# Kernel tuning notes

Hardware: AMD Instinct MI355X
Metric: run time of the kernel (lower is better)

The kernel has to match this reference:

```python
import jax, jax.numpy as jnp
import numpy as np

N_GRAPHS = 1000
P = 300                 # nodes per ring graph
N = N_GRAPHS * P        # 300000 nodes
IN_DIM = 2
HID = 128
OUT_DIM = 2


def _ring_edges():
    idx = jnp.arange(N)
    g = idx // P
    pos = idx % P
    nxt = g * P + (pos + 1) % P
    src = jnp.concatenate([idx, nxt])
    dst = jnp.concatenate([nxt, idx])
    return jnp.stack([src, dst]), g


def setup_inputs() -> dict:
    key = jax.random.key(0)
    ks = jax.random.split(key, 11)
    edge_index, batch = _ring_edges()
    x = jax.random.normal(ks[0], (N, IN_DIM), jnp.float32)

    def glorot(k, fan_in, fan_out):
        lim = np.sqrt(6.0 / (fan_in + fan_out)).astype(np.float32)
        return jax.random.uniform(k, (fan_in, fan_out), jnp.float32, -lim, lim)

    return {
        "x": x,
        "edge_index": edge_index,
        "batch": batch,
        "W1": glorot(ks[1], IN_DIM, HID), "b1": jnp.zeros((HID,), jnp.float32),
        "W2": glorot(ks[2], HID, HID),    "b2": jnp.zeros((HID,), jnp.float32),
        "W3": glorot(ks[3], HID, HID),    "b3": jnp.zeros((HID,), jnp.float32),
        "fw1": glorot(ks[4], HID, HID),   "fb1": jnp.zeros((HID,), jnp.float32),
        "fw2": glorot(ks[5], HID, OUT_DIM), "fb2": jnp.zeros((OUT_DIM,), jnp.float32),
    }


def _gcn_conv(x, W, b, src, dst, norm):
    h = x @ W                              # [N, out]
    msg = h[src] * norm[:, None]           # gather + per-edge scale
    agg = jax.ops.segment_sum(msg, dst, num_segments=N)  # scatter-add
    return agg + b


def reference(x, edge_index, batch, W1, b1, W2, b2, W3, b3, fw1, fb1, fw2, fb2):
    loop = jnp.arange(N)
    src = jnp.concatenate([edge_index[0], loop])
    dst = jnp.concatenate([edge_index[1], loop])
    deg = jax.ops.segment_sum(jnp.ones_like(dst, jnp.float32), dst, num_segments=N)
    dis = jax.lax.rsqrt(deg)               # deg >= 1 due to self-loops
    norm = dis[src] * dis[dst]             # per-edge normalization

    h = jax.nn.relu(_gcn_conv(x, W1, b1, src, dst, norm))
    h = jax.nn.relu(_gcn_conv(h, W2, b2, src, dst, norm))
    h = jax.nn.relu(_gcn_conv(h, W3, b3, src, dst, norm))

    # global mean pool per graph
    sums = jax.ops.segment_sum(h, batch, num_segments=N_GRAPHS)
    cnts = jax.ops.segment_sum(jnp.ones((N,), jnp.float32), batch, num_segments=N_GRAPHS)
    pooled = sums / cnts[:, None]

    out = jax.nn.relu(pooled @ fw1 + fb1)
    out = out @ fw2 + fb2
    return out
```

## Files before the change

kernel.cpp:

```cpp
#include <hip/hip_runtime.h>
#include <hip/hip_bf16.h>
#include <stdint.h>

#define P    300
#define HID  128
#define NG   1000
#define NTL  19

typedef __attribute__((ext_vector_type(8))) short bf16x8;
typedef __attribute__((ext_vector_type(4))) float f32x4;

__device__ short g_wsw[2 * HID * HID];

__device__ __forceinline__ short f2bf(float f) {
    union { float f; uint32_t u; } v; v.f = f;
    uint32_t r = v.u + 0x7fffu + ((v.u >> 16) & 1u);
    return (short)(r >> 16);
}
__device__ __forceinline__ uint32_t pkbf2(float a, float b) {
    union { __hip_bfloat162 h; uint32_t u; } cv;
    cv.h = __float22bfloat162_rn(float2{a, b});
    return cv.u;
}

__global__ __launch_bounds__(256) void k_prep(const float* __restrict__ W2,
                                              const float* __restrict__ W3) {
    int b = blockIdx.x;
    const float* W = (b < 8) ? W2 : W3;
    short* dst = g_wsw + ((b < 8) ? 0 : HID * HID);
    int t    = (b & 7) * 256 + threadIdx.x;
    int fkey = t >> 4;
    int kc   = t & 15;
    bf16x8 o;
    #pragma unroll
    for (int j = 0; j < 8; ++j)
        o[j] = f2bf(W[(kc * 8 + j) * HID + fkey]);
    *(bf16x8*)&dst[(fkey * 16 + (kc ^ (fkey & 15))) * 8] = o;
}

__device__ __forceinline__ void avg_epi(const f32x4 &G, float vp0, float vn3,
                                        float b, float* o) {
    o[0] = (vp0  + G[0] + G[1]) * (1.0f / 3.0f) + b;
    o[1] = (G[0] + G[1] + G[2]) * (1.0f / 3.0f) + b;
    o[2] = (G[1] + G[2] + G[3]) * (1.0f / 3.0f) + b;
    o[3] = (G[2] + G[3] + vn3 ) * (1.0f / 3.0f) + b;
    #pragma unroll
    for (int i = 0; i < 4; ++i) o[i] = o[i] > 0.f ? o[i] : 0.f;
}

template<int POOL>
__device__ __forceinline__ void run_pass(short* __restrict__ buf,
                                         const short* __restrict__ wbase,
                                         const float* __restrict__ bias,
                                         float* __restrict__ pool, int tid) {
    const int lane = tid & 63, wv = tid >> 6, q = lane >> 4, lm = lane & 15;
    const int fkey = wv * 16 + lm;
    bf16x8 wf[4];
    #pragma unroll
    for (int kk = 0; kk < 4; ++kk)
        wf[kk] = *(const bf16x8*)&wbase[(fkey * 16 + ((4 * kk + q) ^ lm)) * 8];
    const float biaf = bias[fkey];
    const int kcs = fkey >> 3, offs = fkey & 7;
    const int sA = (q == 0) ? (48 + lm) : (lane - 16);
    const int sB = (lane + 16) & 63;

    float psum = 0.f;

    auto mfma_tile = [&](int t, f32x4 &G) {
        const short* tb = buf + t * 2048;
        G = f32x4{0.f, 0.f, 0.f, 0.f};
        #pragma unroll
        for (int kk = 0; kk < 4; ++kk) {
            bf16x8 af = *(const bf16x8*)&tb[(lm * 16 + ((4 * kk + q) ^ lm)) * 8];
            G = __builtin_amdgcn_mfma_f32_16x16x32_bf16(af, wf[kk], G, 0, 0, 0);
        }
    };
    auto store_rows = [&](int T, float (&o)[4]) {
        uint32_t u01 = pkbf2(o[0], o[1]);
        uint32_t u23 = pkbf2(o[2], o[3]);
        int n0 = T * 16 + q * 4;
        buf[(n0 * 16       + (kcs ^ ( n0      & 15))) * 8 + offs] = (short)u01;
        buf[((n0 + 1) * 16 + (kcs ^ ((n0 + 1) & 15))) * 8 + offs] = (short)(u01 >> 16);
        buf[((n0 + 2) * 16 + (kcs ^ ((n0 + 2) & 15))) * 8 + offs] = (short)u23;
        buf[((n0 + 3) * 16 + (kcs ^ ((n0 + 3) & 15))) * 8 + offs] = (short)(u23 >> 16);
    };
    auto accum = [&](float (&o)[4]) { psum += o[0] + o[1] + o[2] + o[3]; };

    float c15;
    auto epi_mid = [&](const f32x4 &E, float N0, float (&o)[4]) {
        float vA = __shfl(E[3], sA, 64);
        float vB = __shfl(E[0], sB, 64);
        float vC = __shfl(N0, lm, 64);
        float vp0 = (q == 0) ? c15 : vA;
        float vn3 = (q == 3) ? vC : vB;
        avg_epi(E, vp0, vn3, biaf, o);
        c15 = vA;
    };

    f32x4 GH[10];
    f32x4 GL[9];

    #pragma unroll
    for (int k = 0; k < 9; ++k) mfma_tile(10 + k, GH[k]);
    mfma_tile(0, GH[9]);
    if (!POOL) __syncthreads();

    #pragma unroll
    for (int i = 0; i < 9; ++i) {
        mfma_tile(9 - i, GL[i]);
        if (i == 0) c15 = __shfl(GL[0][3], 48 + lm, 64);
        if (i < 8) {
            float o[4];
            epi_mid(GH[i], GH[i + 1][0], o);
            if (POOL) accum(o); else store_rows(10 + i, o);
        } else {
            float o18[4];
            {
                float vA = __shfl(GH[8][3], sA, 64);
                float vB = __shfl(GH[8][0], sB, 64);
                float vZ = __shfl(GH[9][0], lm, 64);
                float vp0 = (q == 0) ? c15 : vA;
                float vn3 = (q == 2) ? vZ : vB;
                avg_epi(GH[8], vp0, vn3, biaf, o18);
            }
            if (q < 3) { if (POOL) accum(o18); else store_rows(18, o18); }
            float o0[4];
            {
                float vA0 = __shfl(GH[9][3], (lane - 16) & 63, 64);
                float vB0 = __shfl(GH[9][0], sB, 64);
                float vP  = __shfl(GH[8][3], 32 + lm, 64);
                float vN  = __shfl(GL[8][0], lm, 64);
                float vp0 = (q == 0) ? vP : vA0;
                float vn3 = (q == 3) ? vN : vB0;
                avg_epi(GH[9], vp0, vn3, biaf, o0);
            }
            if (POOL) accum(o0); else store_rows(0, o0);
        }
    }
    if (!POOL) __syncthreads();

    c15 = __shfl(GH[9][3], 48 + lm, 64);
    #pragma unroll
    for (int T = 1; T <= 9; ++T) {
        float o[4];
        float N0 = (T < 9) ? GL[8 - T][0] : GH[0][0];
        epi_mid(GL[9 - T], N0, o);
        if (POOL) accum(o); else store_rows(T, o);
    }

    if (POOL) {
        psum += __shfl_xor(psum, 16, 64);
        psum += __shfl_xor(psum, 32, 64);
        if (q == 0) pool[fkey] = psum;
    }
}

__global__ __launch_bounds__(512, 2) void k_graph(
        const float* __restrict__ x,
        const float* __restrict__ W1,  const float* __restrict__ b1,
        const float* __restrict__ b2v, const float* __restrict__ b3v,
        const float* __restrict__ fw1, const float* __restrict__ fb1,
        const float* __restrict__ fw2, const float* __restrict__ fb2,
        float* __restrict__ out) {
    __shared__ __align__(16) short buf[304 * HID];
    __shared__ __align__(16) float scr[640];
    float* xs    = scr;
    float* pool  = scr;
    float* parts = scr + 128;
    float* s1    = scr + 384;

    const int g = blockIdx.x, tid = threadIdx.x;

    if (tid < 150) *(float4*)&xs[tid * 4] = *(const float4*)&x[g * 600 + tid * 4];
    __syncthreads();

    {
        const int kc1 = tid & 15;
        const int n0  = tid >> 4;
        float w1x[8], w1y[8], b1v[8];
        #pragma unroll
        for (int j = 0; j < 8; ++j) {
            w1x[j] = W1[kc1 * 8 + j];
            w1y[j] = W1[HID + kc1 * 8 + j];
            b1v[j] = b1[kc1 * 8 + j];
        }
        #pragma unroll
        for (int it = 0; it < 10; ++it) {
            int node = it * 32 + n0;
            if (node < 304) {
                uint32_t w[4] = {0u, 0u, 0u, 0u};
                if (node < P) {
                    int prev = (node == 0)     ? P - 1 : node - 1;
                    int next = (node == P - 1) ? 0     : node + 1;
                    float2 xp = *(const float2*)&xs[2 * prev];
                    float2 xc = *(const float2*)&xs[2 * node];
                    float2 xn = *(const float2*)&xs[2 * next];
                    float ax = (xp.x + xc.x + xn.x) * (1.f / 3.f);
                    float ay = (xp.y + xc.y + xn.y) * (1.f / 3.f);
                    #pragma unroll
                    for (int jj = 0; jj < 4; ++jj) {
                        float va = ax * w1x[2*jj]   + ay * w1y[2*jj]   + b1v[2*jj];
                        float vb = ax * w1x[2*jj+1] + ay * w1y[2*jj+1] + b1v[2*jj+1];
                        va = va > 0.f ? va : 0.f;
                        vb = vb > 0.f ? vb : 0.f;
                        w[jj] = pkbf2(va, vb);
                    }
                }
                *(uint4*)&buf[(node * 16 + (kc1 ^ (node & 15))) * 8] =
                    uint4{w[0], w[1], w[2], w[3]};
            }
        }
    }
    __syncthreads();

    run_pass<0>(buf, g_wsw,             b2v, pool, tid);
    __syncthreads();
    run_pass<1>(buf, g_wsw + HID * HID, b3v, pool, tid);
    __syncthreads();

    if (tid < 256) {
        int f = tid & 127, half = tid >> 7;
        float p = 0.f;
        const float* fw1c = fw1 + f;
        #pragma unroll 4
        for (int k = half * 64; k < half * 64 + 64; ++k)
            p += pool[k] * fw1c[k * 128];
        parts[half * 128 + f] = p;
    }
    __syncthreads();
    if (tid < 128) {
        float o1 = fb1[tid] + (parts[tid] + parts[128 + tid]) * (1.0f / 300.0f);
        s1[tid] = o1 > 0.f ? o1 : 0.f;
    }
    __syncthreads();
    if (tid < 128) {
        int o = tid >> 6, ln = tid & 63;
        float v = s1[ln] * fw2[ln * 2 + o] + s1[ln + 64] * fw2[(ln + 64) * 2 + o];
        #pragma unroll
        for (int off = 1; off <= 32; off <<= 1)
            v += __shfl_xor(v, off, 64);
        if (ln == 0) out[g * 2 + o] = v + fb2[o];
    }
}

extern "C" void kernel_launch(void* const* d_in, const int* in_sizes, int n_in,
                              void* d_out, int out_size, void* d_ws, size_t ws_size,
                              hipStream_t stream) {
    const float* x   = (const float*)d_in[0];
    const float* W1  = (const float*)d_in[3];
    const float* b1  = (const float*)d_in[4];
    const float* W2  = (const float*)d_in[5];
    const float* b2  = (const float*)d_in[6];
    const float* W3  = (const float*)d_in[7];
    const float* b3  = (const float*)d_in[8];
    const float* fw1 = (const float*)d_in[9];
    const float* fb1 = (const float*)d_in[10];
    const float* fw2 = (const float*)d_in[11];
    const float* fb2 = (const float*)d_in[12];
    float* out = (float*)d_out;

    k_prep <<<dim3(16), dim3(256), 0, stream>>>(W2, W3);
    k_graph<<<dim3(NG), dim3(512), 0, stream>>>(x, W1, b1, b2, b3,
                                                fw1, fb1, fw2, fb2, out);
}
```

Measured before the change: 121.6 us.

## Split each ring graph across two blocks with halo rows and separate FC kernel

```diff
diff --git a/kernel.cpp b/kernel.cpp
--- a/kernel.cpp
+++ b/kernel.cpp
@@ -5,12 +5,13 @@
 #define P    300
 #define HID  128
 #define NG   1000
-#define NTL  19
+#define HR   160
 
 typedef __attribute__((ext_vector_type(8))) short bf16x8;
 typedef __attribute__((ext_vector_type(4))) float f32x4;
 
 __device__ short g_wsw[2 * HID * HID];
+__device__ float g_pool[NG * 2 * HID];
 
 __device__ __forceinline__ short f2bf(float f) {
     union { float f; uint32_t u; } v; v.f = f;
@@ -48,7 +49,7 @@
     for (int i = 0; i < 4; ++i) o[i] = o[i] > 0.f ? o[i] : 0.f;
 }
 
-template<int POOL>
+template<int POOL, int LO, int HI>
 __device__ __forceinline__ void run_pass(short* __restrict__ buf,
                                          const short* __restrict__ wbase,
                                          const float* __restrict__ bias,
@@ -78,15 +79,24 @@
     auto store_rows = [&](int T, float (&o)[4]) {
         uint32_t u01 = pkbf2(o[0], o[1]);
         uint32_t u23 = pkbf2(o[2], o[3]);
-        int n0 = T * 16 + q * 4;
-        buf[(n0 * 16       + (kcs ^ ( n0      & 15))) * 8 + offs] = (short)u01;
-        buf[((n0 + 1) * 16 + (kcs ^ ((n0 + 1) & 15))) * 8 + offs] = (short)(u01 >> 16);
-        buf[((n0 + 2) * 16 + (kcs ^ ((n0 + 2) & 15))) * 8 + offs] = (short)u23;
-        buf[((n0 + 3) * 16 + (kcs ^ ((n0 + 3) & 15))) * 8 + offs] = (short)(u23 >> 16);
-    };
-    auto accum = [&](float (&o)[4]) { psum += o[0] + o[1] + o[2] + o[3]; };
-
-    float c15;
+        int r0 = T * 16 + q * 4;
+        if (r0     >= LO && r0     <= HI)
+            buf[(r0 * 16       + (kcs ^ ( r0      & 15))) * 8 + offs] = (short)u01;
+        if (r0 + 1 >= LO && r0 + 1 <= HI)
+            buf[((r0 + 1) * 16 + (kcs ^ ((r0 + 1) & 15))) * 8 + offs] = (short)(u01 >> 16);
+        if (r0 + 2 >= LO && r0 + 2 <= HI)
+            buf[((r0 + 2) * 16 + (kcs ^ ((r0 + 2) & 15))) * 8 + offs] = (short)u23;
+        if (r0 + 3 >= LO && r0 + 3 <= HI)
+            buf[((r0 + 3) * 16 + (kcs ^ ((r0 + 3) & 15))) * 8 + offs] = (short)(u23 >> 16);
+    };
+    auto accum = [&](int T, float (&o)[4]) {
+        int r0 = T * 16 + q * 4;
+        #pragma unroll
+        for (int i = 0; i < 4; ++i)
+            if (r0 + i >= LO && r0 + i <= HI) psum += o[i];
+    };
+
+    float c15 = 0.f;
     auto epi_mid = [&](const f32x4 &E, float N0, float (&o)[4]) {
         float vA = __shfl(E[3], sA, 64);
         float vB = __shfl(E[0], sB, 64);
@@ -97,55 +107,31 @@
         c15 = vA;
     };
 
-    f32x4 GH[10];
-    f32x4 GL[9];
-
-    #pragma unroll
-    for (int k = 0; k < 9; ++k) mfma_tile(10 + k, GH[k]);
-    mfma_tile(0, GH[9]);
+    f32x4 GH[5];
+    f32x4 GL[5];
+
+    #pragma unroll
+    for (int k = 0; k < 5; ++k) mfma_tile(5 + k, GH[k]);
     if (!POOL) __syncthreads();
 
     #pragma unroll
-    for (int i = 0; i < 9; ++i) {
-        mfma_tile(9 - i, GL[i]);
+    for (int i = 0; i < 5; ++i) {
+        mfma_tile(4 - i, GL[i]);
         if (i == 0) c15 = __shfl(GL[0][3], 48 + lm, 64);
-        if (i < 8) {
-            float o[4];
-            epi_mid(GH[i], GH[i + 1][0], o);
-            if (POOL) accum(o); else store_rows(10 + i, o);
-        } else {
-            float o18[4];
-            {
-                float vA = __shfl(GH[8][3], sA, 64);
-                float vB = __shfl(GH[8][0], sB, 64);
-                float vZ = __shfl(GH[9][0], lm, 64);
-                float vp0 = (q == 0) ? c15 : vA;
-                float vn3 = (q == 2) ? vZ : vB;
-                avg_epi(GH[8], vp0, vn3, biaf, o18);
-            }
-            if (q < 3) { if (POOL) accum(o18); else store_rows(18, o18); }
-            float o0[4];
-            {
-                float vA0 = __shfl(GH[9][3], (lane - 16) & 63, 64);
-                float vB0 = __shfl(GH[9][0], sB, 64);
-                float vP  = __shfl(GH[8][3], 32 + lm, 64);
-                float vN  = __shfl(GL[8][0], lm, 64);
-                float vp0 = (q == 0) ? vP : vA0;
-                float vn3 = (q == 3) ? vN : vB0;
-                avg_epi(GH[9], vp0, vn3, biaf, o0);
-            }
-            if (POOL) accum(o0); else store_rows(0, o0);
-        }
+        float o[4];
+        float N0 = (i < 4) ? GH[i + 1][0] : GH[4][0];
+        epi_mid(GH[i], N0, o);
+        if (POOL) accum(5 + i, o); else store_rows(5 + i, o);
     }
     if (!POOL) __syncthreads();
 
-    c15 = __shfl(GH[9][3], 48 + lm, 64);
-    #pragma unroll
-    for (int T = 1; T <= 9; ++T) {
+    c15 = 0.f;
+    #pragma unroll
+    for (int k = 0; k < 5; ++k) {
         float o[4];
-        float N0 = (T < 9) ? GL[8 - T][0] : GH[0][0];
-        epi_mid(GL[9 - T], N0, o);
-        if (POOL) accum(o); else store_rows(T, o);
+        float N0 = (k < 4) ? GL[3 - k][0] : GH[0][0];
+        epi_mid(GL[4 - k], N0, o);
+        if (POOL) accum(k, o); else store_rows(k, o);
     }
 
     if (POOL) {
@@ -158,20 +144,19 @@
 __global__ __launch_bounds__(512, 2) void k_graph(
         const float* __restrict__ x,
         const float* __restrict__ W1,  const float* __restrict__ b1,
-        const float* __restrict__ b2v, const float* __restrict__ b3v,
-        const float* __restrict__ fw1, const float* __restrict__ fb1,
-        const float* __restrict__ fw2, const float* __restrict__ fb2,
-        float* __restrict__ out) {
-    __shared__ __align__(16) short buf[304 * HID];
-    __shared__ __align__(16) float scr[640];
-    float* xs    = scr;
-    float* pool  = scr;
-    float* parts = scr + 128;
-    float* s1    = scr + 384;
-
-    const int g = blockIdx.x, tid = threadIdx.x;
-
-    if (tid < 150) *(float4*)&xs[tid * 4] = *(const float4*)&x[g * 600 + tid * 4];
+        const float* __restrict__ b2v, const float* __restrict__ b3v) {
+    __shared__ __align__(16) short buf[HR * HID];
+    __shared__ __align__(16) float xs[316];
+    const int bid = blockIdx.x, g = bid >> 1, half = bid & 1;
+    const int tid = threadIdx.x;
+    const int start = half * 150;
+
+    if (tid < 156) {
+        int gn = start - 3 + tid;
+        gn += (gn < 0) ? P : 0;
+        gn -= (gn >= P) ? P : 0;
+        *(float2*)&xs[2 * tid] = *(const float2*)&x[g * 600 + gn * 2];
+    }
     __syncthreads();
 
     {
@@ -185,62 +170,57 @@
             b1v[j] = b1[kc1 * 8 + j];
         }
         #pragma unroll
-        for (int it = 0; it < 10; ++it) {
-            int node = it * 32 + n0;
-            if (node < 304) {
-                uint32_t w[4] = {0u, 0u, 0u, 0u};
-                if (node < P) {
-                    int prev = (node == 0)     ? P - 1 : node - 1;
-                    int next = (node == P - 1) ? 0     : node + 1;
-                    float2 xp = *(const float2*)&xs[2 * prev];
-                    float2 xc = *(const float2*)&xs[2 * node];
-                    float2 xn = *(const float2*)&xs[2 * next];
-                    float ax = (xp.x + xc.x + xn.x) * (1.f / 3.f);
-                    float ay = (xp.y + xc.y + xn.y) * (1.f / 3.f);
-                    #pragma unroll
-                    for (int jj = 0; jj < 4; ++jj) {
-                        float va = ax * w1x[2*jj]   + ay * w1y[2*jj]   + b1v[2*jj];
-                        float vb = ax * w1x[2*jj+1] + ay * w1y[2*jj+1] + b1v[2*jj+1];
-                        va = va > 0.f ? va : 0.f;
-                        vb = vb > 0.f ? vb : 0.f;
-                        w[jj] = pkbf2(va, vb);
-                    }
+        for (int it = 0; it < 5; ++it) {
+            int row = it * 32 + n0;
+            uint32_t w[4] = {0u, 0u, 0u, 0u};
+            if (row < 154) {
+                float2 xp = *(const float2*)&xs[2 * row];
+                float2 xc = *(const float2*)&xs[2 * row + 2];
+                float2 xn = *(const float2*)&xs[2 * row + 4];
+                float ax = (xp.x + xc.x + xn.x) * (1.f / 3.f);
+                float ay = (xp.y + xc.y + xn.y) * (1.f / 3.f);
+                #pragma unroll
+                for (int jj = 0; jj < 4; ++jj) {
+                    float va = ax * w1x[2*jj]   + ay * w1y[2*jj]   + b1v[2*jj];
+                    float vb = ax * w1x[2*jj+1] + ay * w1y[2*jj+1] + b1v[2*jj+1];
+                    va = va > 0.f ? va : 0.f;
+                    vb = vb > 0.f ? vb : 0.f;
+                    w[jj] = pkbf2(va, vb);
                 }
-                *(uint4*)&buf[(node * 16 + (kc1 ^ (node & 15))) * 8] =
-                    uint4{w[0], w[1], w[2], w[3]};
             }
+            *(uint4*)&buf[(row * 16 + (kc1 ^ (row & 15))) * 8] =
+                uint4{w[0], w[1], w[2], w[3]};
         }
     }
     __syncthreads();
 
-    run_pass<0>(buf, g_wsw,             b2v, pool, tid);
-    __syncthreads();
-    run_pass<1>(buf, g_wsw + HID * HID, b3v, pool, tid);
-    __syncthreads();
-
-    if (tid < 256) {
-        int f = tid & 127, half = tid >> 7;
-        float p = 0.f;
-        const float* fw1c = fw1 + f;
-        #pragma unroll 4
-        for (int k = half * 64; k < half * 64 + 64; ++k)
-            p += pool[k] * fw1c[k * 128];
-        parts[half * 128 + f] = p;
-    }
-    __syncthreads();
-    if (tid < 128) {
-        float o1 = fb1[tid] + (parts[tid] + parts[128 + tid]) * (1.0f / 300.0f);
-        s1[tid] = o1 > 0.f ? o1 : 0.f;
-    }
-    __syncthreads();
-    if (tid < 128) {
-        int o = tid >> 6, ln = tid & 63;
-        float v = s1[ln] * fw2[ln * 2 + o] + s1[ln + 64] * fw2[(ln + 64) * 2 + o];
-        #pragma unroll
-        for (int off = 1; off <= 32; off <<= 1)
-            v += __shfl_xor(v, off, 64);
-        if (ln == 0) out[g * 2 + o] = v + fb2[o];
-    }
+    run_pass<0, 1, 152>(buf, g_wsw,             b2v, nullptr, tid);
+    __syncthreads();
+    run_pass<1, 2, 151>(buf, g_wsw + HID * HID, b3v,
+                        &g_pool[(g * 2 + half) * HID], tid);
+}
+
+__global__ __launch_bounds__(128) void k_fc(
+        const float* __restrict__ fw1, const float* __restrict__ fb1,
+        const float* __restrict__ fw2, const float* __restrict__ fb2,
+        float* __restrict__ out) {
+    __shared__ float pl[128], s1[128];
+    const int g = blockIdx.x, f = threadIdx.x;
+    pl[f] = g_pool[g * 256 + f] + g_pool[g * 256 + 128 + f];
+    __syncthreads();
+    float p = 0.f;
+    const float* c = fw1 + f;
+    #pragma unroll 8
+    for (int k = 0; k < 128; ++k) p += pl[k] * c[k * 128];
+    float o1 = fb1[f] + p * (1.0f / 300.0f);
+    s1[f] = o1 > 0.f ? o1 : 0.f;
+    __syncthreads();
+    int o = f >> 6, ln = f & 63;
+    float v = s1[ln] * fw2[ln * 2 + o] + s1[ln + 64] * fw2[(ln + 64) * 2 + o];
+    #pragma unroll
+    for (int off = 1; off <= 32; off <<= 1)
+        v += __shfl_xor(v, off, 64);
+    if (ln == 0) out[g * 2 + o] = v + fb2[o];
 }
 
 extern "C" void kernel_launch(void* const* d_in, const int* in_sizes, int n_in,
@@ -259,7 +239,7 @@
     const float* fb2 = (const float*)d_in[12];
     float* out = (float*)d_out;
 
-    k_prep <<<dim3(16), dim3(256), 0, stream>>>(W2, W3);
-    k_graph<<<dim3(NG), dim3(512), 0, stream>>>(x, W1, b1, b2, b3,
-                                                fw1, fb1, fw2, fb2, out);
-}
+    k_prep <<<dim3(16),     dim3(256), 0, stream>>>(W2, W3);
+    k_graph<<<dim3(2 * NG), dim3(512), 0, stream>>>(x, W1, b1, b2, b3);
+    k_fc   <<<dim3(NG),     dim3(128), 0, stream>>>(fw1, fb1, fw2, fb2, out);
+}
```

After: 126.3 us. +3.9%, slower.
